# Kernel tuning notes

Measured on AMD Instinct MI355X. Metric: run time of the kernel, lower is better.

The kernel has to match this reference:

```python
import jax, jax.numpy as jnp
import numpy as np

B, T, U = 32, 1024, 1024


def setup_inputs() -> dict:
    key = jax.random.key(0)
    k0, k1, k2, k3 = jax.random.split(key, 4)
    x = jax.random.normal(k0, (B, T, U), dtype=jnp.float32)
    w_gates = jax.random.normal(k1, (4 * U,), dtype=jnp.float32) * 0.1
    b_gates = jax.random.normal(k2, (4 * U,), dtype=jnp.float32) * 0.1
    w_dense = jax.random.normal(k3, (U, 1), dtype=jnp.float32) * 0.02
    b_dense = jnp.zeros((1,), dtype=jnp.float32)
    return {"x": x, "w_gates": w_gates, "b_gates": b_gates,
            "w_dense": w_dense, "b_dense": b_dense}


def reference(x, w_gates, b_gates, w_dense, b_dense):
    # x: [B, T, U]; gates are elementwise per-channel (faithful to source,
    # which multiplies kernel slices elementwise with inputs; gates do NOT
    # depend on h_{t-1}).
    u = x.shape[-1]
    wi, wf, wg, wo = (w_gates[:u], w_gates[u:2*u], w_gates[2*u:3*u], w_gates[3*u:])
    bi, bf, bg, bo = (b_gates[:u], b_gates[u:2*u], b_gates[2*u:3*u], b_gates[3*u:])

    def step(carry, x_t):  # x_t: [B, U]
        h, c = carry
        i = jax.nn.sigmoid(wi * x_t + bi)
        f = jax.nn.sigmoid(wf * x_t + bf)
        g = jnp.tanh(wg * x_t + bg)
        o = jax.nn.sigmoid(wo * x_t + bo)
        c = f * c + i * g
        h = o * jnp.tanh(c)
        return (h, c), None

    b = x.shape[0]
    h0 = jnp.zeros((b, u), dtype=x.dtype)
    c0 = jnp.zeros((b, u), dtype=x.dtype)
    (h, _), _ = jax.lax.scan(step, (h0, c0), jnp.swapaxes(x, 0, 1))  # scan over T
    return h @ w_dense + b_dense  # [B, 1]
```

## Files before the change

### kernel.cpp

```cpp
#include <hip/hip_runtime.h>

#define BB 32
#define TT 1024
#define UU 1024
#define CHUNKS 32
#define LCH (TT / CHUNKS)
#define U4 (UU / 4)

#define LOG2E 1.44269504088896340736f

__device__ __forceinline__ float fast_rcp(float x)  { return __builtin_amdgcn_rcpf(x); }
__device__ __forceinline__ float fast_exp2(float x) { return __builtin_amdgcn_exp2f(x); }

__device__ __forceinline__ float sig_pre(float wp, float x, float bp) {
    return fast_rcp(1.0f + fast_exp2(fmaf(wp, x, bp)));
}
__device__ __forceinline__ float tanh_pre(float wp, float x, float bp) {
    return fmaf(-2.0f, fast_rcp(1.0f + fast_exp2(fmaf(wp, x, bp))), 1.0f);
}

__device__ __forceinline__ void step1(float xv,
                                      float wi, float bi, float wf, float bf,
                                      float wg, float bg, float& F, float& P) {
    const float ig = sig_pre(wi, xv, bi);
    const float fg = sig_pre(wf, xv, bf);
    const float gg = tanh_pre(wg, xv, bg);
    P = fmaf(fg, P, ig * gg);
    F *= fg;
}

__global__ __launch_bounds__(256) void lstm_chunk_kernel(
    const float4* __restrict__ x,
    const float4* __restrict__ w_gates,
    const float4* __restrict__ b_gates,
    float4* __restrict__ Fout,
    float4* __restrict__ Pout)
{
    const int idx   = blockIdx.x * 256 + threadIdx.x;
    const int u4    = idx & (U4 - 1);
    const int b     = (idx >> 8) & (BB - 1);
    const int chunk = idx >> 13;

    float4 wi = w_gates[u4];
    float4 wf = w_gates[U4 + u4];
    float4 wg = w_gates[2 * U4 + u4];
    float4 bi = b_gates[u4];
    float4 bf = b_gates[U4 + u4];
    float4 bg = b_gates[2 * U4 + u4];
    wi.x *= -LOG2E; wi.y *= -LOG2E; wi.z *= -LOG2E; wi.w *= -LOG2E;
    bi.x *= -LOG2E; bi.y *= -LOG2E; bi.z *= -LOG2E; bi.w *= -LOG2E;
    wf.x *= -LOG2E; wf.y *= -LOG2E; wf.z *= -LOG2E; wf.w *= -LOG2E;
    bf.x *= -LOG2E; bf.y *= -LOG2E; bf.z *= -LOG2E; bf.w *= -LOG2E;
    wg.x *= 2*LOG2E; wg.y *= 2*LOG2E; wg.z *= 2*LOG2E; wg.w *= 2*LOG2E;
    bg.x *= 2*LOG2E; bg.y *= 2*LOG2E; bg.z *= 2*LOG2E; bg.w *= 2*LOG2E;

    const float4* xp = x + ((size_t)b * TT + (size_t)chunk * LCH) * U4 + u4;

    float4 F = make_float4(1.f, 1.f, 1.f, 1.f);
    float4 P = make_float4(0.f, 0.f, 0.f, 0.f);
#pragma unroll 8
    for (int j = 0; j < LCH; ++j) {
        const float4 xv = xp[(size_t)j * U4];
        step1(xv.x, wi.x, bi.x, wf.x, bf.x, wg.x, bg.x, F.x, P.x);
        step1(xv.y, wi.y, bi.y, wf.y, bf.y, wg.y, bg.y, F.y, P.y);
        step1(xv.z, wi.z, bi.z, wf.z, bf.z, wg.z, bg.z, F.z, P.z);
        step1(xv.w, wi.w, bi.w, wf.w, bf.w, wg.w, bg.w, F.w, P.w);
    }
    Fout[idx] = F;
    Pout[idx] = P;
}

__global__ __launch_bounds__(256) void lstm_final_kernel(
    const float4* __restrict__ Fin,
    const float4* __restrict__ Pin,
    const float4* __restrict__ x,
    const float4* __restrict__ w_gates,
    const float4* __restrict__ b_gates,
    const float4* __restrict__ w_dense,
    const float* __restrict__ b_dense,
    float* __restrict__ out)
{
    const int b   = blockIdx.x;
    const int tid = threadIdx.x;

    float4 c = make_float4(0.f, 0.f, 0.f, 0.f);
#pragma unroll
    for (int ch = 0; ch < CHUNKS; ++ch) {
        const size_t o = (size_t)ch * BB * U4 + (size_t)b * U4 + tid;
        const float4 F = Fin[o];
        const float4 P = Pin[o];
        c.x = fmaf(F.x, c.x, P.x);
        c.y = fmaf(F.y, c.y, P.y);
        c.z = fmaf(F.z, c.z, P.z);
        c.w = fmaf(F.w, c.w, P.w);
    }

    const float4 xv = x[((size_t)b * TT + (TT - 1)) * U4 + tid];
    float4 wo = w_gates[3 * U4 + tid];
    float4 bo = b_gates[3 * U4 + tid];
    wo.x *= -LOG2E; wo.y *= -LOG2E; wo.z *= -LOG2E; wo.w *= -LOG2E;
    bo.x *= -LOG2E; bo.y *= -LOG2E; bo.z *= -LOG2E; bo.w *= -LOG2E;
    const float4 wd = w_dense[tid];

    float sum;
    {
        const float hx = sig_pre(wo.x, xv.x, bo.x) *
                         fmaf(-2.0f, fast_rcp(1.0f + fast_exp2(2.f * LOG2E * c.x)), 1.0f);
        const float hy = sig_pre(wo.y, xv.y, bo.y) *
                         fmaf(-2.0f, fast_rcp(1.0f + fast_exp2(2.f * LOG2E * c.y)), 1.0f);
        const float hz = sig_pre(wo.z, xv.z, bo.z) *
                         fmaf(-2.0f, fast_rcp(1.0f + fast_exp2(2.f * LOG2E * c.z)), 1.0f);
        const float hw = sig_pre(wo.w, xv.w, bo.w) *
                         fmaf(-2.0f, fast_rcp(1.0f + fast_exp2(2.f * LOG2E * c.w)), 1.0f);
        sum = hx * wd.x + hy * wd.y + hz * wd.z + hw * wd.w;
    }

    __shared__ float red[256];
    red[tid] = sum;
    __syncthreads();
#pragma unroll
    for (int s = 128; s > 0; s >>= 1) {
        if (tid < s) red[tid] += red[tid + s];
        __syncthreads();
    }
    if (tid == 0) out[b] = red[0] + b_dense[0];
}

extern "C" void kernel_launch(void* const* d_in, const int* in_sizes, int n_in,
                              void* d_out, int out_size, void* d_ws, size_t ws_size,
                              hipStream_t stream) {
    const float4* x       = (const float4*)d_in[0];
    const float4* w_gates = (const float4*)d_in[1];
    const float4* b_gates = (const float4*)d_in[2];
    const float4* w_dense = (const float4*)d_in[3];
    const float* b_dense  = (const float*)d_in[4];
    float* out = (float*)d_out;

    float4* Fout = (float4*)d_ws;
    float4* Pout = (float4*)((char*)d_ws + (size_t)CHUNKS * BB * UU * 4);

    const int total = CHUNKS * BB * U4;
    lstm_chunk_kernel<<<total / 256, 256, 0, stream>>>(x, w_gates, b_gates, Fout, Pout);
    lstm_final_kernel<<<BB, 256, 0, stream>>>(Fout, Pout, x, w_gates, b_gates,
                                              w_dense, b_dense, out);
}
```

Before: 205.4 us.

## Reformulate chunk recurrence with deferred division and double chunk count

Rewrites the per-step gate math so the forget-gate product and partial cell are kept as an unnormalized numerator/denominator pair. This cuts the per-step reciprocals from three to one, with a single reciprocal at chunk end to recover F and P. Chunk count doubles, which raises parallelism but doubles workspace traffic and the length of the final combine loop. The running product D of (1+Ef) terms could overflow for long chunks or large gate inputs, which is a numerical risk.

After: 221.0 us. 1.08x slower.

```diff
diff --git a/kernel.cpp b/kernel.cpp
--- a/kernel.cpp
+++ b/kernel.cpp
@@ -3,7 +3,7 @@
 #define BB 32
 #define TT 1024
 #define UU 1024
-#define CHUNKS 32
+#define CHUNKS 64
 #define LCH (TT / CHUNKS)
 #define U4 (UU / 4)
 
@@ -12,21 +12,23 @@
 __device__ __forceinline__ float fast_rcp(float x)  { return __builtin_amdgcn_rcpf(x); }
 __device__ __forceinline__ float fast_exp2(float x) { return __builtin_amdgcn_exp2f(x); }
 
-__device__ __forceinline__ float sig_pre(float wp, float x, float bp) {
-    return fast_rcp(1.0f + fast_exp2(fmaf(wp, x, bp)));
-}
-__device__ __forceinline__ float tanh_pre(float wp, float x, float bp) {
-    return fmaf(-2.0f, fast_rcp(1.0f + fast_exp2(fmaf(wp, x, bp))), 1.0f);
+__device__ __forceinline__ float Eexp(float wp, float x, float bp) {
+    return fast_exp2(fmaf(wp, x, bp));
 }
 
 __device__ __forceinline__ void step1(float xv,
                                       float wi, float bi, float wf, float bf,
-                                      float wg, float bg, float& F, float& P) {
-    const float ig = sig_pre(wi, xv, bi);
-    const float fg = sig_pre(wf, xv, bf);
-    const float gg = tanh_pre(wg, xv, bg);
-    P = fmaf(fg, P, ig * gg);
-    F *= fg;
+                                      float wg, float bg, float& D, float& Q) {
+    const float Ei = Eexp(wi, xv, bi);
+    const float Ef = Eexp(wf, xv, bf);
+    const float Eg = Eexp(wg, xv, bg);
+    const float ti = 1.0f + Ei;
+    const float tf = 1.0f + Ef;
+    const float tgp = 1.0f + Eg;
+    const float tgm = 1.0f - Eg;
+    const float r  = tgm * fast_rcp(ti * tgp);
+    D *= tf;
+    Q = fmaf(r, D, Q);
 }
 
 __global__ __launch_bounds__(256) void lstm_chunk_kernel(
@@ -47,25 +49,28 @@
     float4 bi = b_gates[u4];
     float4 bf = b_gates[U4 + u4];
     float4 bg = b_gates[2 * U4 + u4];
-    wi.x *= -LOG2E; wi.y *= -LOG2E; wi.z *= -LOG2E; wi.w *= -LOG2E;
-    bi.x *= -LOG2E; bi.y *= -LOG2E; bi.z *= -LOG2E; bi.w *= -LOG2E;
-    wf.x *= -LOG2E; wf.y *= -LOG2E; wf.z *= -LOG2E; wf.w *= -LOG2E;
-    bf.x *= -LOG2E; bf.y *= -LOG2E; bf.z *= -LOG2E; bf.w *= -LOG2E;
-    wg.x *= 2*LOG2E; wg.y *= 2*LOG2E; wg.z *= 2*LOG2E; wg.w *= 2*LOG2E;
-    bg.x *= 2*LOG2E; bg.y *= 2*LOG2E; bg.z *= 2*LOG2E; bg.w *= 2*LOG2E;
+    wi.x *= -LOG2E;   wi.y *= -LOG2E;   wi.z *= -LOG2E;   wi.w *= -LOG2E;
+    bi.x *= -LOG2E;   bi.y *= -LOG2E;   bi.z *= -LOG2E;   bi.w *= -LOG2E;
+    wf.x *= -LOG2E;   wf.y *= -LOG2E;   wf.z *= -LOG2E;   wf.w *= -LOG2E;
+    bf.x *= -LOG2E;   bf.y *= -LOG2E;   bf.z *= -LOG2E;   bf.w *= -LOG2E;
+    wg.x *= -2*LOG2E; wg.y *= -2*LOG2E; wg.z *= -2*LOG2E; wg.w *= -2*LOG2E;
+    bg.x *= -2*LOG2E; bg.y *= -2*LOG2E; bg.z *= -2*LOG2E; bg.w *= -2*LOG2E;
 
     const float4* xp = x + ((size_t)b * TT + (size_t)chunk * LCH) * U4 + u4;
 
-    float4 F = make_float4(1.f, 1.f, 1.f, 1.f);
-    float4 P = make_float4(0.f, 0.f, 0.f, 0.f);
+    float4 D = make_float4(1.f, 1.f, 1.f, 1.f);
+    float4 Q = make_float4(0.f, 0.f, 0.f, 0.f);
 #pragma unroll 8
     for (int j = 0; j < LCH; ++j) {
         const float4 xv = xp[(size_t)j * U4];
-        step1(xv.x, wi.x, bi.x, wf.x, bf.x, wg.x, bg.x, F.x, P.x);
-        step1(xv.y, wi.y, bi.y, wf.y, bf.y, wg.y, bg.y, F.y, P.y);
-        step1(xv.z, wi.z, bi.z, wf.z, bf.z, wg.z, bg.z, F.z, P.z);
-        step1(xv.w, wi.w, bi.w, wf.w, bf.w, wg.w, bg.w, F.w, P.w);
+        step1(xv.x, wi.x, bi.x, wf.x, bf.x, wg.x, bg.x, D.x, Q.x);
+        step1(xv.y, wi.y, bi.y, wf.y, bf.y, wg.y, bg.y, D.y, Q.y);
+        step1(xv.z, wi.z, bi.z, wf.z, bf.z, wg.z, bg.z, D.z, Q.z);
+        step1(xv.w, wi.w, bi.w, wf.w, bf.w, wg.w, bg.w, D.w, Q.w);
     }
+    float4 F, P;
+    F.x = fast_rcp(D.x); F.y = fast_rcp(D.y); F.z = fast_rcp(D.z); F.w = fast_rcp(D.w);
+    P.x = Q.x * F.x;     P.y = Q.y * F.y;     P.z = Q.z * F.z;     P.w = Q.w * F.w;
     Fout[idx] = F;
     Pout[idx] = P;
 }
@@ -102,18 +107,15 @@
     bo.x *= -LOG2E; bo.y *= -LOG2E; bo.z *= -LOG2E; bo.w *= -LOG2E;
     const float4 wd = w_dense[tid];
 
-    float sum;
-    {
-        const float hx = sig_pre(wo.x, xv.x, bo.x) *
-                         fmaf(-2.0f, fast_rcp(1.0f + fast_exp2(2.f * LOG2E * c.x)), 1.0f);
-        const float hy = sig_pre(wo.y, xv.y, bo.y) *
-                         fmaf(-2.0f, fast_rcp(1.0f + fast_exp2(2.f * LOG2E * c.y)), 1.0f);
-        const float hz = sig_pre(wo.z, xv.z, bo.z) *
-                         fmaf(-2.0f, fast_rcp(1.0f + fast_exp2(2.f * LOG2E * c.z)), 1.0f);
-        const float hw = sig_pre(wo.w, xv.w, bo.w) *
-                         fmaf(-2.0f, fast_rcp(1.0f + fast_exp2(2.f * LOG2E * c.w)), 1.0f);
-        sum = hx * wd.x + hy * wd.y + hz * wd.z + hw * wd.w;
-    }
+    const float hx = fast_rcp(1.0f + fast_exp2(fmaf(wo.x, xv.x, bo.x))) *
+                     fmaf(-2.0f, fast_rcp(1.0f + fast_exp2(2.f * LOG2E * c.x)), 1.0f);
+    const float hy = fast_rcp(1.0f + fast_exp2(fmaf(wo.y, xv.y, bo.y))) *
+                     fmaf(-2.0f, fast_rcp(1.0f + fast_exp2(2.f * LOG2E * c.y)), 1.0f);
+    const float hz = fast_rcp(1.0f + fast_exp2(fmaf(wo.z, xv.z, bo.z))) *
+                     fmaf(-2.0f, fast_rcp(1.0f + fast_exp2(2.f * LOG2E * c.z)), 1.0f);
+    const float hw = fast_rcp(1.0f + fast_exp2(fmaf(wo.w, xv.w, bo.w))) *
+                     fmaf(-2.0f, fast_rcp(1.0f + fast_exp2(2.f * LOG2E * c.w)), 1.0f);
+    const float sum = hx * wd.x + hy * wd.y + hz * wd.z + hw * wd.w;
 
     __shared__ float red[256];
     red[tid] = sum;
```
